# Kernel optimization log

Hardware: AMD Instinct MI355X
Metric: run time of the kernel (lower is better)

Reference implementation:

```python
import jax, jax.numpy as jnp
import numpy as np

E, R, K, D, B = 100000, 1000, 200, 256, 65536  # entities, relations, bundle heads, emb dim, batch


def setup_inputs() -> dict:
    key = jax.random.key(0)
    ks = jax.random.split(key, 12)
    ent_emb = jax.random.normal(ks[0], (E, D), dtype=jnp.float32)
    ent_emb = ent_emb / jnp.linalg.norm(ent_emb, axis=1, keepdims=True)  # xavier + L2 row-normalize
    heads = jax.random.normal(ks[1], (K, D), dtype=jnp.float32)
    heads = heads / jnp.linalg.norm(heads, axis=1, keepdims=True)  # normalize_vvrel_embeddings
    bases = jax.random.normal(ks[2], (R, 2, D), dtype=jnp.float32)
    bases = bases / jnp.linalg.norm(bases, axis=2, keepdims=True)  # normalize_all_rows
    rel2head = jax.random.randint(ks[3], (R,), 0, K)              # r_id2_vrr[rel][0] -> head idx
    rel2mult = jnp.where(jax.random.bernoulli(ks[4], 0.5, (R,)), 1.0, -1.0).astype(jnp.float32)  # r_id2_vrr[rel][1]
    return {
        'pos_h': jax.random.randint(ks[5], (B,), 0, E),
        'pos_t': jax.random.randint(ks[6], (B,), 0, E),
        'pos_r': jax.random.randint(ks[7], (B,), 0, R),
        'neg_h': jax.random.randint(ks[8], (B,), 0, E),
        'neg_t': jax.random.randint(ks[9], (B,), 0, E),
        'neg_r': jax.random.randint(ks[10], (B,), 0, R),
        'ent_emb': ent_emb, 'heads': heads, 'bases': bases,
        'rel2head': rel2head, 'rel2mult': rel2mult,
    }


def _transint_scores(pos_h, pos_t, pos_r, neg_h, neg_t, ent_emb, heads, bases, rel2head, rel2mult):
    # vvrel_embedding_func: head embedding scaled by +-1 multiplier
    r_e = heads[rel2head[pos_r]] * rel2mult[pos_r][:, None]           # [B, D]
    pos_sub = ent_emb[pos_h] + r_e - ent_emb[pos_t]                    # [B, D]
    neg_sub = ent_emb[neg_h] + r_e - ent_emb[neg_t]                    # [B, D] (note: uses pos_r_e, as in source)
    sub = jnp.concatenate([pos_sub, neg_sub], axis=0)                  # [2B, D]
    A = bases[jnp.concatenate([pos_r, pos_r], axis=0)]                 # [2B, 2, D] per-sample basis (comb_mats gather)
    # ATA and closed-form 2x2 inverse (module's `inverse`)
    ATA = jnp.einsum('bkd,bld->bkl', A, A)                             # [2B, 2, 2]
    a, b = ATA[:, 0, 0], ATA[:, 0, 1]
    c, d = ATA[:, 1, 0], ATA[:, 1, 1]
    det = a * d - b * c
    safe_det = jnp.where(det != 0, det, 1.0)
    inv_reg = jnp.stack([jnp.stack([d, -b], -1), jnp.stack([-c, a], -1)], -2) / safe_det[:, None, None]
    inv_fb = jnp.eye(2, dtype=ATA.dtype)[None] / a[:, None, None]      # fallback when det == 0
    ATA_inv = jnp.where((det != 0)[:, None, None], inv_reg, inv_fb)    # [2B, 2, 2]
    # P @ sub with P = I - A^T (A A^T)^{-1} A, applied without materializing P
    Asub = jnp.einsum('bkd,bd->bk', A, sub)                            # [2B, 2]
    proj = sub - jnp.einsum('bkd,bk->bd', A, jnp.einsum('bkl,bl->bk', ATA_inv, Asub))
    score = jnp.sum(proj ** 2, axis=1)                                 # L1_flag = False -> squared L2
    nb = pos_h.shape[0]
    return score[:nb], score[nb:]


def reference(pos_h, pos_t, pos_r, neg_h, neg_t, neg_r, ent_emb, heads, bases, rel2head, rel2mult):
    return _transint_scores(pos_h, pos_t, pos_r, neg_h, neg_t, ent_emb, heads, bases, rel2head, rel2mult)
```

## Files before the change

### kernel.cpp

```cpp
#include <hip/hip_runtime.h>

#define D 256
#define D4 (D/4)
#define RELQW 192

#define QSCALE (1.0f/254.0f)
#define QINV   254.0f
#define QS2    (QSCALE*QSCALE)

__device__ inline float dot4(const float4 u, const float4 v) {
    return u.x*v.x + u.y*v.y + u.z*v.z + u.w*v.w;
}

__device__ inline float wsum(float v) {
    #pragma unroll
    for (int off = 32; off > 0; off >>= 1)
        v += __shfl_xor(v, off, 64);
    return v;
}

__device__ inline void unpack_i8(unsigned w, int* f) {
    f[0] = (int)(w << 24) >> 24;
    f[1] = (int)(w << 16) >> 24;
    f[2] = (int)(w <<  8) >> 24;
    f[3] = (int)w         >> 24;
}

__device__ inline int q8(float v) {
    float q = rintf(v * QINV);
    q = fmaxf(-127.f, fminf(127.f, q));
    return (int)q;
}

__device__ inline unsigned pack4q(float a, float b, float c, float d) {
    return (unsigned)(q8(a) & 255)
         | ((unsigned)(q8(b) & 255) << 8)
         | ((unsigned)(q8(c) & 255) << 16)
         | ((unsigned)(q8(d) & 255) << 24);
}

__global__ __launch_bounds__(256) void transint_prep(
    const float*  __restrict__ ent,
    const float*  __restrict__ heads,
    const float*  __restrict__ bases,
    const int*    __restrict__ rel2head,
    const float*  __restrict__ rel2mult,
    unsigned*     __restrict__ ent_q,
    unsigned*     __restrict__ rel_q,
    float*        __restrict__ par_buf,
    int E, int R)
{
    const int wave = (blockIdx.x * blockDim.x + threadIdx.x) >> 6;
    const int lane = threadIdx.x & 63;

    if (wave < E) {
        float4 v = ((const float4*)ent)[(size_t)wave * D4 + lane];
        ent_q[(size_t)wave * 64 + lane] = pack4q(v.x, v.y, v.z, v.w);
        return;
    }
    const int r = wave - E;
    if (r >= R) return;

    const int hd = rel2head[r];
    const float mult = rel2mult[r];
    const float4* hrow = (const float4*)(heads + (size_t)hd * D);
    const float4* arow = (const float4*)(bases + (size_t)r * 2 * D);

    float4 a0 = arow[lane];
    float4 a1 = arow[D4 + lane];
    float4 re = hrow[lane];
    re.x *= mult; re.y *= mult; re.z *= mult; re.w *= mult;

    float aa = wsum(dot4(a0, a0));
    float ab = wsum(dot4(a0, a1));
    float dd = wsum(dot4(a1, a1));

    float det = aa * dd - ab * ab;
    float m00, m01, m11;
    if (det != 0.0f) {
        float inv = 1.0f / det;
        m00 = dd * inv; m01 = -ab * inv; m11 = aa * inv;
    } else {
        float inv = 1.0f / aa;
        m00 = inv; m01 = 0.0f; m11 = inv;
    }
    float t00 = aa * m00 + ab * m01;
    float t01 = aa * m01 + ab * m11;
    float t10 = ab * m00 + dd * m01;
    float t11 = ab * m01 + dd * m11;
    float q00 = 2.f * m00 - (m00 * t00 + m01 * t10);
    float q01 = 2.f * m01 - (m00 * t01 + m01 * t11);
    float q11 = 2.f * m11 - (m01 * t01 + m11 * t11);

    float c00 = sqrtf(aa);
    float ic00 = (c00 > 0.f) ? 1.f / c00 : 0.f;
    float4 u0;
    u0.x = a0.x * ic00; u0.y = a0.y * ic00; u0.z = a0.z * ic00; u0.w = a0.w * ic00;
    float c10 = ab * ic00;
    float4 v;
    v.x = a1.x - c10 * u0.x; v.y = a1.y - c10 * u0.y;
    v.z = a1.z - c10 * u0.z; v.w = a1.w - c10 * u0.w;
    float vv = wsum(dot4(v, v));
    float c11 = sqrtf(vv);
    float ic11 = (c11 > 0.f) ? 1.f / c11 : 0.f;
    float4 u1;
    u1.x = v.x * ic11; u1.y = v.y * ic11; u1.z = v.z * ic11; u1.w = v.w * ic11;

    float s00 = c00*c00*q00 + 2.f*c00*c10*q01 + c10*c10*q11;
    float s01 = c00*c11*q01 + c10*c11*q11;
    float s11 = c11*c11*q11;

    unsigned* base = rel_q + (size_t)r * RELQW;
    base[lane]       = pack4q(u0.x, u0.y, u0.z, u0.w);
    base[64 + lane]  = pack4q(u1.x, u1.y, u1.z, u1.w);
    base[128 + lane] = pack4q(re.x, re.y, re.z, re.w);

    if (lane == 0) {
        float* p = par_buf + (size_t)r * 4;
        p[0] = s00; p[1] = s01; p[2] = s11; p[3] = 0.f;
    }
}

__global__ __launch_bounds__(256) void transint_main(
    const int*      __restrict__ pos_h,
    const int*      __restrict__ pos_t,
    const int*      __restrict__ pos_r,
    const int*      __restrict__ neg_h,
    const int*      __restrict__ neg_t,
    const unsigned* __restrict__ ent_q,
    const unsigned* __restrict__ rel_q,
    const float*    __restrict__ par_buf,
    float*          __restrict__ out,
    int nB)
{
    const int wave = (blockIdx.x * blockDim.x + threadIdx.x) >> 6;
    const int lane = threadIdx.x & 63;
    const int g    = lane >> 4;
    const int gl   = lane & 15;
    const int base = wave * 8;
    int bs[2];
    bs[0] = base + g;
    bs[1] = base + 4 + g;
    if (bs[0] >= nB) return;
    const bool has1 = (bs[1] < nB);
    if (!has1) bs[1] = bs[0];

    const int4* eq = (const int4*)ent_q;
    const int4* rq = (const int4*)rel_q;

    int rr[2];
    const int4 *php[2], *ptp[2], *nhp[2], *ntp[2], *rbp[2];

    #pragma unroll
    for (int s = 0; s < 2; ++s) {
        const int b = bs[s];
        rr[s] = pos_r[b];
        php[s] = eq + (size_t)pos_h[b] * 16;
        ptp[s] = eq + (size_t)pos_t[b] * 16;
        nhp[s] = eq + (size_t)neg_h[b] * 16;
        ntp[s] = eq + (size_t)neg_t[b] * 16;
        rbp[s] = rq + (size_t)rr[s] * 48;
    }

    int pp0[2] = {0,0}, pp1[2] = {0,0};
    int pn0[2] = {0,0}, pn1[2] = {0,0};
    int ssp[2] = {0,0}, ssn[2] = {0,0};

    #pragma unroll
    for (int s = 0; s < 2; ++s) {
        int4 qh  = php[s][gl];
        int4 qt  = ptp[s][gl];
        int4 qx  = nhp[s][gl];
        int4 qy  = ntp[s][gl];
        int4 qu0 = rbp[s][gl];
        int4 qu1 = rbp[s][gl + 16];
        int4 qre = rbp[s][gl + 32];

        const unsigned* hw  = (const unsigned*)&qh;
        const unsigned* tw  = (const unsigned*)&qt;
        const unsigned* xw  = (const unsigned*)&qx;
        const unsigned* yw  = (const unsigned*)&qy;
        const unsigned* u0w = (const unsigned*)&qu0;
        const unsigned* u1w = (const unsigned*)&qu1;
        const unsigned* rw  = (const unsigned*)&qre;

        #pragma unroll
        for (int w = 0; w < 4; ++w) {
            int h4[4], t4[4], x4[4], y4[4], a4[4], b4[4], r4[4];
            unpack_i8(hw[w],  h4);
            unpack_i8(tw[w],  t4);
            unpack_i8(xw[w],  x4);
            unpack_i8(yw[w],  y4);
            unpack_i8(u0w[w], a4);
            unpack_i8(u1w[w], b4);
            unpack_i8(rw[w],  r4);
            #pragma unroll
            for (int j = 0; j < 4; ++j) {
                int ps = h4[j] - t4[j] + r4[j];
                int ns = x4[j] - y4[j] + r4[j];
                pp0[s] += a4[j] * ps;
                pp1[s] += b4[j] * ps;
                pn0[s] += a4[j] * ns;
                pn1[s] += b4[j] * ns;
                ssp[s] += ps * ps;
                ssn[s] += ns * ns;
            }
        }
    }

    #pragma unroll
    for (int off = 8; off > 0; off >>= 1) {
        #pragma unroll
        for (int s = 0; s < 2; ++s) {
            pp0[s] += __shfl_xor(pp0[s], off, 64);
            pp1[s] += __shfl_xor(pp1[s], off, 64);
            pn0[s] += __shfl_xor(pn0[s], off, 64);
            pn1[s] += __shfl_xor(pn1[s], off, 64);
            ssp[s] += __shfl_xor(ssp[s], off, 64);
            ssn[s] += __shfl_xor(ssn[s], off, 64);
        }
    }

    if (gl == 0) {
        #pragma unroll
        for (int s = 0; s < 2; ++s) {
            if (s == 1 && !has1) break;
            const float* par = par_buf + (size_t)rr[s] * 4;
            const float s00 = par[0], s01 = par[1], s11 = par[2];
            float P0 = (float)pp0[s] * QS2;
            float P1 = (float)pp1[s] * QS2;
            float N0 = (float)pn0[s] * QS2;
            float N1 = (float)pn1[s] * QS2;
            float SP = (float)ssp[s] * QS2;
            float SN = (float)ssn[s] * QS2;
            float sp = SP - (s00*P0*P0 + 2.f*s01*P0*P1 + s11*P1*P1);
            float sn = SN - (s00*N0*N0 + 2.f*s01*N0*N1 + s11*N1*N1);
            out[bs[s]]      = sp;
            out[nB + bs[s]] = sn;
        }
    }
}

extern "C" void kernel_launch(void* const* d_in, const int* in_sizes, int n_in,
                              void* d_out, int out_size, void* d_ws, size_t ws_size,
                              hipStream_t stream) {
    const int*   pos_h    = (const int*)  d_in[0];
    const int*   pos_t    = (const int*)  d_in[1];
    const int*   pos_r    = (const int*)  d_in[2];
    const int*   neg_h    = (const int*)  d_in[3];
    const int*   neg_t    = (const int*)  d_in[4];
    const float* ent_emb  = (const float*)d_in[6];
    const float* heads    = (const float*)d_in[7];
    const float* bases    = (const float*)d_in[8];
    const int*   rel2head = (const int*)  d_in[9];
    const float* rel2mult = (const float*)d_in[10];
    float* out = (float*)d_out;

    const int nB = in_sizes[0];
    const int R  = in_sizes[9];
    const int E  = in_sizes[6] / D;

    unsigned* ent_q   = (unsigned*)d_ws;
    unsigned* rel_q   = (unsigned*)((char*)d_ws + (size_t)E * 256);
    float*    par_buf = (float*)(rel_q + (size_t)R * RELQW);

    {
        int waves = E + R;
        dim3 grid((waves + 3) / 4);
        transint_prep<<<grid, dim3(256), 0, stream>>>(
            ent_emb, heads, bases, rel2head, rel2mult,
            ent_q, rel_q, par_buf, E, R);
    }
    {
        dim3 grid((nB + 31) / 32);
        transint_main<<<grid, dim3(256), 0, stream>>>(
            pos_h, pos_t, pos_r, neg_h, neg_t,
            ent_q, rel_q, par_buf, out, nB);
    }
}
```

Baseline: 187.6 us.

## Drop per-call int8 entity quantization and gather fp32 embeddings directly

The prep kernel no longer quantizes the whole 100k-row entity table to int8 on every call. It now only precomputes the orthonormal basis, relation vector and 2x2 correction terms per relation, stored in fp32. The main kernel gathers fp32 entity rows directly and accumulates in float, with one sample per 16-lane group. This removes a full read plus write pass over the entity table. In exchange, each gathered row is four times larger, so the random-gather traffic rises, and the kernel relies on the large last-level cache to hold the table.

```diff
diff --git a/kernel.cpp b/kernel.cpp
--- a/kernel.cpp
+++ b/kernel.cpp
@@ -2,11 +2,6 @@
 
 #define D 256
 #define D4 (D/4)
-#define RELQW 192
-
-#define QSCALE (1.0f/254.0f)
-#define QINV   254.0f
-#define QS2    (QSCALE*QSCALE)
 
 __device__ inline float dot4(const float4 u, const float4 v) {
     return u.x*v.x + u.y*v.y + u.z*v.z + u.w*v.w;
@@ -19,49 +14,20 @@
     return v;
 }
 
-__device__ inline void unpack_i8(unsigned w, int* f) {
-    f[0] = (int)(w << 24) >> 24;
-    f[1] = (int)(w << 16) >> 24;
-    f[2] = (int)(w <<  8) >> 24;
-    f[3] = (int)w         >> 24;
-}
-
-__device__ inline int q8(float v) {
-    float q = rintf(v * QINV);
-    q = fmaxf(-127.f, fminf(127.f, q));
-    return (int)q;
-}
-
-__device__ inline unsigned pack4q(float a, float b, float c, float d) {
-    return (unsigned)(q8(a) & 255)
-         | ((unsigned)(q8(b) & 255) << 8)
-         | ((unsigned)(q8(c) & 255) << 16)
-         | ((unsigned)(q8(d) & 255) << 24);
-}
-
-__global__ __launch_bounds__(256) void transint_prep(
-    const float*  __restrict__ ent,
-    const float*  __restrict__ heads,
-    const float*  __restrict__ bases,
-    const int*    __restrict__ rel2head,
-    const float*  __restrict__ rel2mult,
-    unsigned*     __restrict__ ent_q,
-    unsigned*     __restrict__ rel_q,
-    float*        __restrict__ par_buf,
-    int E, int R)
+__global__ __launch_bounds__(256) void transint_relprep(
+    const float* __restrict__ heads,
+    const float* __restrict__ bases,
+    const int*   __restrict__ rel2head,
+    const float* __restrict__ rel2mult,
+    float*       __restrict__ rel_f,
+    float*       __restrict__ par_buf,
+    int R)
 {
-    const int wave = (blockIdx.x * blockDim.x + threadIdx.x) >> 6;
+    const int r    = (blockIdx.x * blockDim.x + threadIdx.x) >> 6;
     const int lane = threadIdx.x & 63;
-
-    if (wave < E) {
-        float4 v = ((const float4*)ent)[(size_t)wave * D4 + lane];
-        ent_q[(size_t)wave * 64 + lane] = pack4q(v.x, v.y, v.z, v.w);
-        return;
-    }
-    const int r = wave - E;
     if (r >= R) return;
 
-    const int hd = rel2head[r];
+    const int   hd   = rel2head[r];
     const float mult = rel2mult[r];
     const float4* hrow = (const float4*)(heads + (size_t)hd * D);
     const float4* arow = (const float4*)(bases + (size_t)r * 2 * D);
@@ -92,7 +58,7 @@
     float q01 = 2.f * m01 - (m00 * t01 + m01 * t11);
     float q11 = 2.f * m11 - (m01 * t01 + m11 * t11);
 
-    float c00 = sqrtf(aa);
+    float c00  = sqrtf(aa);
     float ic00 = (c00 > 0.f) ? 1.f / c00 : 0.f;
     float4 u0;
     u0.x = a0.x * ic00; u0.y = a0.y * ic00; u0.z = a0.z * ic00; u0.w = a0.w * ic00;
@@ -100,8 +66,8 @@
     float4 v;
     v.x = a1.x - c10 * u0.x; v.y = a1.y - c10 * u0.y;
     v.z = a1.z - c10 * u0.z; v.w = a1.w - c10 * u0.w;
-    float vv = wsum(dot4(v, v));
-    float c11 = sqrtf(vv);
+    float vv   = wsum(dot4(v, v));
+    float c11  = sqrtf(vv);
     float ic11 = (c11 > 0.f) ? 1.f / c11 : 0.f;
     float4 u1;
     u1.x = v.x * ic11; u1.y = v.y * ic11; u1.z = v.z * ic11; u1.w = v.w * ic11;
@@ -110,10 +76,10 @@
     float s01 = c00*c11*q01 + c10*c11*q11;
     float s11 = c11*c11*q11;
 
-    unsigned* base = rel_q + (size_t)r * RELQW;
-    base[lane]       = pack4q(u0.x, u0.y, u0.z, u0.w);
-    base[64 + lane]  = pack4q(u1.x, u1.y, u1.z, u1.w);
-    base[128 + lane] = pack4q(re.x, re.y, re.z, re.w);
+    float4* rf = (float4*)(rel_f + (size_t)r * 3 * D);
+    rf[lane]          = u0;
+    rf[D4 + lane]     = u1;
+    rf[2 * D4 + lane] = re;
 
     if (lane == 0) {
         float* p = par_buf + (size_t)r * 4;
@@ -121,123 +87,78 @@
     }
 }
 
-__global__ __launch_bounds__(256) void transint_main(
-    const int*      __restrict__ pos_h,
-    const int*      __restrict__ pos_t,
-    const int*      __restrict__ pos_r,
-    const int*      __restrict__ neg_h,
-    const int*      __restrict__ neg_t,
-    const unsigned* __restrict__ ent_q,
-    const unsigned* __restrict__ rel_q,
-    const float*    __restrict__ par_buf,
-    float*          __restrict__ out,
+__global__ __launch_bounds__(256) void transint_main_f32(
+    const int*   __restrict__ pos_h,
+    const int*   __restrict__ pos_t,
+    const int*   __restrict__ pos_r,
+    const int*   __restrict__ neg_h,
+    const int*   __restrict__ neg_t,
+    const float* __restrict__ ent,
+    const float* __restrict__ rel_f,
+    const float* __restrict__ par_buf,
+    float*       __restrict__ out,
     int nB)
 {
     const int wave = (blockIdx.x * blockDim.x + threadIdx.x) >> 6;
     const int lane = threadIdx.x & 63;
     const int g    = lane >> 4;
     const int gl   = lane & 15;
-    const int base = wave * 8;
-    int bs[2];
-    bs[0] = base + g;
-    bs[1] = base + 4 + g;
-    if (bs[0] >= nB) return;
-    const bool has1 = (bs[1] < nB);
-    if (!has1) bs[1] = bs[0];
+    const int b    = wave * 4 + g;
+    if (b >= nB) return;
 
-    const int4* eq = (const int4*)ent_q;
-    const int4* rq = (const int4*)rel_q;
+    const int r = pos_r[b];
+    const float4* ph = (const float4*)ent + (size_t)pos_h[b] * D4;
+    const float4* pt = (const float4*)ent + (size_t)pos_t[b] * D4;
+    const float4* nh = (const float4*)ent + (size_t)neg_h[b] * D4;
+    const float4* nt = (const float4*)ent + (size_t)neg_t[b] * D4;
+    const float4* rb = (const float4*)rel_f + (size_t)r * (3 * D4);
 
-    int rr[2];
-    const int4 *php[2], *ptp[2], *nhp[2], *ntp[2], *rbp[2];
+    float4 H[4], T[4], X[4], Y[4], U0[4], U1[4], RE[4];
+    #pragma unroll
+    for (int c = 0; c < 4; ++c) {
+        const int fi = gl + 16 * c;
+        H[c]  = ph[fi];
+        T[c]  = pt[fi];
+        X[c]  = nh[fi];
+        Y[c]  = nt[fi];
+        U0[c] = rb[fi];
+        U1[c] = rb[D4 + fi];
+        RE[c] = rb[2 * D4 + fi];
+    }
+
+    float pp0 = 0.f, pp1 = 0.f, ssp = 0.f;
+    float pn0 = 0.f, pn1 = 0.f, ssn = 0.f;
 
     #pragma unroll
-    for (int s = 0; s < 2; ++s) {
-        const int b = bs[s];
-        rr[s] = pos_r[b];
-        php[s] = eq + (size_t)pos_h[b] * 16;
-        ptp[s] = eq + (size_t)pos_t[b] * 16;
-        nhp[s] = eq + (size_t)neg_h[b] * 16;
-        ntp[s] = eq + (size_t)neg_t[b] * 16;
-        rbp[s] = rq + (size_t)rr[s] * 48;
-    }
-
-    int pp0[2] = {0,0}, pp1[2] = {0,0};
-    int pn0[2] = {0,0}, pn1[2] = {0,0};
-    int ssp[2] = {0,0}, ssn[2] = {0,0};
-
-    #pragma unroll
-    for (int s = 0; s < 2; ++s) {
-        int4 qh  = php[s][gl];
-        int4 qt  = ptp[s][gl];
-        int4 qx  = nhp[s][gl];
-        int4 qy  = ntp[s][gl];
-        int4 qu0 = rbp[s][gl];
-        int4 qu1 = rbp[s][gl + 16];
-        int4 qre = rbp[s][gl + 32];
-
-        const unsigned* hw  = (const unsigned*)&qh;
-        const unsigned* tw  = (const unsigned*)&qt;
-        const unsigned* xw  = (const unsigned*)&qx;
-        const unsigned* yw  = (const unsigned*)&qy;
-        const unsigned* u0w = (const unsigned*)&qu0;
-        const unsigned* u1w = (const unsigned*)&qu1;
-        const unsigned* rw  = (const unsigned*)&qre;
-
-        #pragma unroll
-        for (int w = 0; w < 4; ++w) {
-            int h4[4], t4[4], x4[4], y4[4], a4[4], b4[4], r4[4];
-            unpack_i8(hw[w],  h4);
-            unpack_i8(tw[w],  t4);
-            unpack_i8(xw[w],  x4);
-            unpack_i8(yw[w],  y4);
-            unpack_i8(u0w[w], a4);
-            unpack_i8(u1w[w], b4);
-            unpack_i8(rw[w],  r4);
-            #pragma unroll
-            for (int j = 0; j < 4; ++j) {
-                int ps = h4[j] - t4[j] + r4[j];
-                int ns = x4[j] - y4[j] + r4[j];
-                pp0[s] += a4[j] * ps;
-                pp1[s] += b4[j] * ps;
-                pn0[s] += a4[j] * ns;
-                pn1[s] += b4[j] * ns;
-                ssp[s] += ps * ps;
-                ssn[s] += ns * ns;
-            }
-        }
+    for (int c = 0; c < 4; ++c) {
+        #define ACC(comp) {                                   \
+            float ps = H[c].comp - T[c].comp + RE[c].comp;    \
+            float ns = X[c].comp - Y[c].comp + RE[c].comp;    \
+            pp0 = fmaf(U0[c].comp, ps, pp0);                  \
+            pp1 = fmaf(U1[c].comp, ps, pp1);                  \
+            ssp = fmaf(ps, ps, ssp);                          \
+            pn0 = fmaf(U0[c].comp, ns, pn0);                  \
+            pn1 = fmaf(U1[c].comp, ns, pn1);                  \
+            ssn = fmaf(ns, ns, ssn); }
+        ACC(x) ACC(y) ACC(z) ACC(w)
+        #undef ACC
     }
 
     #pragma unroll
     for (int off = 8; off > 0; off >>= 1) {
-        #pragma unroll
-        for (int s = 0; s < 2; ++s) {
-            pp0[s] += __shfl_xor(pp0[s], off, 64);
-            pp1[s] += __shfl_xor(pp1[s], off, 64);
-            pn0[s] += __shfl_xor(pn0[s], off, 64);
-            pn1[s] += __shfl_xor(pn1[s], off, 64);
-            ssp[s] += __shfl_xor(ssp[s], off, 64);
-            ssn[s] += __shfl_xor(ssn[s], off, 64);
-        }
+        pp0 += __shfl_xor(pp0, off, 64);
+        pp1 += __shfl_xor(pp1, off, 64);
+        ssp += __shfl_xor(ssp, off, 64);
+        pn0 += __shfl_xor(pn0, off, 64);
+        pn1 += __shfl_xor(pn1, off, 64);
+        ssn += __shfl_xor(ssn, off, 64);
     }
 
     if (gl == 0) {
-        #pragma unroll
-        for (int s = 0; s < 2; ++s) {
-            if (s == 1 && !has1) break;
-            const float* par = par_buf + (size_t)rr[s] * 4;
-            const float s00 = par[0], s01 = par[1], s11 = par[2];
-            float P0 = (float)pp0[s] * QS2;
-            float P1 = (float)pp1[s] * QS2;
-            float N0 = (float)pn0[s] * QS2;
-            float N1 = (float)pn1[s] * QS2;
-            float SP = (float)ssp[s] * QS2;
-            float SN = (float)ssn[s] * QS2;
-            float sp = SP - (s00*P0*P0 + 2.f*s01*P0*P1 + s11*P1*P1);
-            float sn = SN - (s00*N0*N0 + 2.f*s01*N0*N1 + s11*N1*N1);
-            out[bs[s]]      = sp;
-            out[nB + bs[s]] = sn;
-        }
+        const float* par = par_buf + (size_t)r * 4;
+        const float s00 = par[0], s01 = par[1], s11 = par[2];
+        out[b]      = ssp - (s00*pp0*pp0 + 2.f*s01*pp0*pp1 + s11*pp1*pp1);
+        out[nB + b] = ssn - (s00*pn0*pn0 + 2.f*s01*pn0*pn1 + s11*pn1*pn1);
     }
 }
 
@@ -258,23 +179,19 @@
 
     const int nB = in_sizes[0];
     const int R  = in_sizes[9];
-    const int E  = in_sizes[6] / D;
 
-    unsigned* ent_q   = (unsigned*)d_ws;
-    unsigned* rel_q   = (unsigned*)((char*)d_ws + (size_t)E * 256);
-    float*    par_buf = (float*)(rel_q + (size_t)R * RELQW);
+    float* rel_f   = (float*)d_ws;
+    float* par_buf = rel_f + (size_t)R * 3 * D;
 
     {
-        int waves = E + R;
-        dim3 grid((waves + 3) / 4);
-        transint_prep<<<grid, dim3(256), 0, stream>>>(
-            ent_emb, heads, bases, rel2head, rel2mult,
-            ent_q, rel_q, par_buf, E, R);
+        dim3 grid((R + 3) / 4);
+        transint_relprep<<<grid, dim3(256), 0, stream>>>(
+            heads, bases, rel2head, rel2mult, rel_f, par_buf, R);
     }
     {
-        dim3 grid((nB + 31) / 32);
-        transint_main<<<grid, dim3(256), 0, stream>>>(
+        dim3 grid((nB + 15) / 16);
+        transint_main_f32<<<grid, dim3(256), 0, stream>>>(
             pos_h, pos_t, pos_r, neg_h, neg_t,
-            ent_q, rel_q, par_buf, out, nB);
+            ent_emb, rel_f, par_buf, out, nB);
     }
 }
```

New measurement: 197.0 us. 1.05x slower.

## Use packed int8 sdot4 dot products with precomputed relation cross terms

Applied to the files above, without the earlier changes.

Replaces the per-byte unpack and scalar multiply-accumulate in the main kernel with packed 4-way int8 dot products (sdot4). The squared norm and projections are expanded algebraically into pairwise dot products. The relation-only terms (u0·r, u1·r, r·r) are precomputed per relation in the prep kernel and stored in a widened parameter buffer. The intent is to cut ALU work in the main kernel. The cost is more sdot4 ops (18 per word instead of 6 sums) and a larger param row.

```diff
diff --git a/kernel.cpp b/kernel.cpp
--- a/kernel.cpp
+++ b/kernel.cpp
@@ -3,6 +3,7 @@
 #define D 256
 #define D4 (D/4)
 #define RELQW 192
+#define PARW 8
 
 #define QSCALE (1.0f/254.0f)
 #define QINV   254.0f
@@ -17,13 +18,6 @@
     for (int off = 32; off > 0; off >>= 1)
         v += __shfl_xor(v, off, 64);
     return v;
-}
-
-__device__ inline void unpack_i8(unsigned w, int* f) {
-    f[0] = (int)(w << 24) >> 24;
-    f[1] = (int)(w << 16) >> 24;
-    f[2] = (int)(w <<  8) >> 24;
-    f[3] = (int)w         >> 24;
 }
 
 __device__ inline int q8(float v) {
@@ -32,12 +26,33 @@
     return (int)q;
 }
 
+__device__ inline unsigned pack_i(const int* q) {
+    return (unsigned)(q[0] & 255)
+         | ((unsigned)(q[1] & 255) << 8)
+         | ((unsigned)(q[2] & 255) << 16)
+         | ((unsigned)(q[3] & 255) << 24);
+}
+
 __device__ inline unsigned pack4q(float a, float b, float c, float d) {
-    return (unsigned)(q8(a) & 255)
-         | ((unsigned)(q8(b) & 255) << 8)
-         | ((unsigned)(q8(c) & 255) << 16)
-         | ((unsigned)(q8(d) & 255) << 24);
-}
+    int q[4] = {q8(a), q8(b), q8(c), q8(d)};
+    return pack_i(q);
+}
+
+#if __has_builtin(__builtin_amdgcn_sdot4)
+__device__ inline int sdot4(int a, int b, int c) {
+    return __builtin_amdgcn_sdot4(a, b, c, false);
+}
+#else
+__device__ inline int sdot4(int a, int b, int c) {
+    #pragma unroll
+    for (int j = 0; j < 4; ++j) {
+        int av = (int)(((unsigned)a) << (24 - 8*j)) >> 24;
+        int bv = (int)(((unsigned)b) << (24 - 8*j)) >> 24;
+        c += av * bv;
+    }
+    return c;
+}
+#endif
 
 __global__ __launch_bounds__(256) void transint_prep(
     const float*  __restrict__ ent,
@@ -61,7 +76,7 @@
     const int r = wave - E;
     if (r >= R) return;
 
-    const int hd = rel2head[r];
+    const int   hd   = rel2head[r];
     const float mult = rel2mult[r];
     const float4* hrow = (const float4*)(heads + (size_t)hd * D);
     const float4* arow = (const float4*)(bases + (size_t)r * 2 * D);
@@ -92,7 +107,7 @@
     float q01 = 2.f * m01 - (m00 * t01 + m01 * t11);
     float q11 = 2.f * m11 - (m01 * t01 + m11 * t11);
 
-    float c00 = sqrtf(aa);
+    float c00  = sqrtf(aa);
     float ic00 = (c00 > 0.f) ? 1.f / c00 : 0.f;
     float4 u0;
     u0.x = a0.x * ic00; u0.y = a0.y * ic00; u0.z = a0.z * ic00; u0.w = a0.w * ic00;
@@ -100,8 +115,8 @@
     float4 v;
     v.x = a1.x - c10 * u0.x; v.y = a1.y - c10 * u0.y;
     v.z = a1.z - c10 * u0.z; v.w = a1.w - c10 * u0.w;
-    float vv = wsum(dot4(v, v));
-    float c11 = sqrtf(vv);
+    float vv   = wsum(dot4(v, v));
+    float c11  = sqrtf(vv);
     float ic11 = (c11 > 0.f) ? 1.f / c11 : 0.f;
     float4 u1;
     u1.x = v.x * ic11; u1.y = v.y * ic11; u1.z = v.z * ic11; u1.w = v.w * ic11;
@@ -110,14 +125,26 @@
     float s01 = c00*c11*q01 + c10*c11*q11;
     float s11 = c11*c11*q11;
 
-    unsigned* base = rel_q + (size_t)r * RELQW;
-    base[lane]       = pack4q(u0.x, u0.y, u0.z, u0.w);
-    base[64 + lane]  = pack4q(u1.x, u1.y, u1.z, u1.w);
-    base[128 + lane] = pack4q(re.x, re.y, re.z, re.w);
+    int qa[4] = {q8(u0.x), q8(u0.y), q8(u0.z), q8(u0.w)};
+    int qb[4] = {q8(u1.x), q8(u1.y), q8(u1.z), q8(u1.w)};
+    int qr[4] = {q8(re.x), q8(re.y), q8(re.z), q8(re.w)};
+
+    unsigned* basep = rel_q + (size_t)r * RELQW;
+    basep[lane]       = pack_i(qa);
+    basep[64 + lane]  = pack_i(qb);
+    basep[128 + lane] = pack_i(qr);
+
+    float du0re = wsum((float)(qa[0]*qr[0] + qa[1]*qr[1] + qa[2]*qr[2] + qa[3]*qr[3]));
+    float du1re = wsum((float)(qb[0]*qr[0] + qb[1]*qr[1] + qb[2]*qr[2] + qb[3]*qr[3]));
+    float drere = wsum((float)(qr[0]*qr[0] + qr[1]*qr[1] + qr[2]*qr[2] + qr[3]*qr[3]));
 
     if (lane == 0) {
-        float* p = par_buf + (size_t)r * 4;
-        p[0] = s00; p[1] = s01; p[2] = s11; p[3] = 0.f;
+        float* p = par_buf + (size_t)r * PARW;
+        p[0] = s00; p[1] = s01; p[2] = s11;
+        p[3] = du0re * QS2;
+        p[4] = du1re * QS2;
+        p[5] = drere * QS2;
+        p[6] = 0.f; p[7] = 0.f;
     }
 }
 
@@ -149,75 +176,70 @@
     const int4* rq = (const int4*)rel_q;
 
     int rr[2];
-    const int4 *php[2], *ptp[2], *nhp[2], *ntp[2], *rbp[2];
+    int4 qh[2], qt[2], qx[2], qy[2], qu0[2], qu1[2], qre[2];
 
     #pragma unroll
     for (int s = 0; s < 2; ++s) {
         const int b = bs[s];
         rr[s] = pos_r[b];
-        php[s] = eq + (size_t)pos_h[b] * 16;
-        ptp[s] = eq + (size_t)pos_t[b] * 16;
-        nhp[s] = eq + (size_t)neg_h[b] * 16;
-        ntp[s] = eq + (size_t)neg_t[b] * 16;
-        rbp[s] = rq + (size_t)rr[s] * 48;
-    }
-
-    int pp0[2] = {0,0}, pp1[2] = {0,0};
-    int pn0[2] = {0,0}, pn1[2] = {0,0};
-    int ssp[2] = {0,0}, ssn[2] = {0,0};
+        qh[s] = eq[(size_t)pos_h[b] * 16 + gl];
+        qt[s] = eq[(size_t)pos_t[b] * 16 + gl];
+        qx[s] = eq[(size_t)neg_h[b] * 16 + gl];
+        qy[s] = eq[(size_t)neg_t[b] * 16 + gl];
+        const int4* rb = rq + (size_t)rr[s] * 48;
+        qu0[s] = rb[gl];
+        qu1[s] = rb[gl + 16];
+        qre[s] = rb[gl + 32];
+    }
+
+    int p0[2], p1[2], sp[2], n0[2], n1[2], sn[2];
 
     #pragma unroll
     for (int s = 0; s < 2; ++s) {
-        int4 qh  = php[s][gl];
-        int4 qt  = ptp[s][gl];
-        int4 qx  = nhp[s][gl];
-        int4 qy  = ntp[s][gl];
-        int4 qu0 = rbp[s][gl];
-        int4 qu1 = rbp[s][gl + 16];
-        int4 qre = rbp[s][gl + 32];
-
-        const unsigned* hw  = (const unsigned*)&qh;
-        const unsigned* tw  = (const unsigned*)&qt;
-        const unsigned* xw  = (const unsigned*)&qx;
-        const unsigned* yw  = (const unsigned*)&qy;
-        const unsigned* u0w = (const unsigned*)&qu0;
-        const unsigned* u1w = (const unsigned*)&qu1;
-        const unsigned* rw  = (const unsigned*)&qre;
+        int u0h=0,u0t=0,u1h=0,u1t=0, hh=0,tt=0,ht=0, hre=0,tre=0;
+        int u0x=0,u0y=0,u1x=0,u1y=0, xx=0,yy=0,xy=0, xre=0,yre=0;
+
+        const int* hw  = (const int*)&qh[s];
+        const int* tw  = (const int*)&qt[s];
+        const int* xw  = (const int*)&qx[s];
+        const int* yw  = (const int*)&qy[s];
+        const int* aw  = (const int*)&qu0[s];
+        const int* bw  = (const int*)&qu1[s];
+        const int* rw  = (const int*)&qre[s];
 
         #pragma unroll
         for (int w = 0; w < 4; ++w) {
-            int h4[4], t4[4], x4[4], y4[4], a4[4], b4[4], r4[4];
-            unpack_i8(hw[w],  h4);
-            unpack_i8(tw[w],  t4);
-            unpack_i8(xw[w],  x4);
-            unpack_i8(yw[w],  y4);
-            unpack_i8(u0w[w], a4);
-            unpack_i8(u1w[w], b4);
-            unpack_i8(rw[w],  r4);
-            #pragma unroll
-            for (int j = 0; j < 4; ++j) {
-                int ps = h4[j] - t4[j] + r4[j];
-                int ns = x4[j] - y4[j] + r4[j];
-                pp0[s] += a4[j] * ps;
-                pp1[s] += b4[j] * ps;
-                pn0[s] += a4[j] * ns;
-                pn1[s] += b4[j] * ns;
-                ssp[s] += ps * ps;
-                ssn[s] += ns * ns;
-            }
+            const int h = hw[w], t = tw[w], x = xw[w], y = yw[w];
+            const int a = aw[w], b2 = bw[w], r2 = rw[w];
+            u0h = sdot4(a,  h, u0h);  u0t = sdot4(a,  t, u0t);
+            u1h = sdot4(b2, h, u1h);  u1t = sdot4(b2, t, u1t);
+            hh  = sdot4(h,  h, hh);   tt  = sdot4(t,  t, tt);
+            ht  = sdot4(h,  t, ht);
+            hre = sdot4(h, r2, hre);  tre = sdot4(t, r2, tre);
+            u0x = sdot4(a,  x, u0x);  u0y = sdot4(a,  y, u0y);
+            u1x = sdot4(b2, x, u1x);  u1y = sdot4(b2, y, u1y);
+            xx  = sdot4(x,  x, xx);   yy  = sdot4(y,  y, yy);
+            xy  = sdot4(x,  y, xy);
+            xre = sdot4(x, r2, xre);  yre = sdot4(y, r2, yre);
         }
+        p0[s] = u0h - u0t;
+        p1[s] = u1h - u1t;
+        sp[s] = hh + tt - 2*ht + 2*hre - 2*tre;
+        n0[s] = u0x - u0y;
+        n1[s] = u1x - u1y;
+        sn[s] = xx + yy - 2*xy + 2*xre - 2*yre;
     }
 
     #pragma unroll
     for (int off = 8; off > 0; off >>= 1) {
         #pragma unroll
         for (int s = 0; s < 2; ++s) {
-            pp0[s] += __shfl_xor(pp0[s], off, 64);
-            pp1[s] += __shfl_xor(pp1[s], off, 64);
-            pn0[s] += __shfl_xor(pn0[s], off, 64);
-            pn1[s] += __shfl_xor(pn1[s], off, 64);
-            ssp[s] += __shfl_xor(ssp[s], off, 64);
-            ssn[s] += __shfl_xor(ssn[s], off, 64);
+            p0[s] += __shfl_xor(p0[s], off, 64);
+            p1[s] += __shfl_xor(p1[s], off, 64);
+            sp[s] += __shfl_xor(sp[s], off, 64);
+            n0[s] += __shfl_xor(n0[s], off, 64);
+            n1[s] += __shfl_xor(n1[s], off, 64);
+            sn[s] += __shfl_xor(sn[s], off, 64);
         }
     }
 
@@ -225,18 +247,17 @@
         #pragma unroll
         for (int s = 0; s < 2; ++s) {
             if (s == 1 && !has1) break;
-            const float* par = par_buf + (size_t)rr[s] * 4;
+            const float* par = par_buf + (size_t)rr[s] * PARW;
             const float s00 = par[0], s01 = par[1], s11 = par[2];
-            float P0 = (float)pp0[s] * QS2;
-            float P1 = (float)pp1[s] * QS2;
-            float N0 = (float)pn0[s] * QS2;
-            float N1 = (float)pn1[s] * QS2;
-            float SP = (float)ssp[s] * QS2;
-            float SN = (float)ssn[s] * QS2;
-            float sp = SP - (s00*P0*P0 + 2.f*s01*P0*P1 + s11*P1*P1);
-            float sn = SN - (s00*N0*N0 + 2.f*s01*N0*N1 + s11*N1*N1);
-            out[bs[s]]      = sp;
-            out[nB + bs[s]] = sn;
+            const float u0re = par[3], u1re = par[4], rere = par[5];
+            float P0 = (float)p0[s] * QS2 + u0re;
+            float P1 = (float)p1[s] * QS2 + u1re;
+            float SP = (float)sp[s] * QS2 + rere;
+            float N0 = (float)n0[s] * QS2 + u0re;
+            float N1 = (float)n1[s] * QS2 + u1re;
+            float SN = (float)sn[s] * QS2 + rere;
+            out[bs[s]]      = SP - (s00*P0*P0 + 2.f*s01*P0*P1 + s11*P1*P1);
+            out[nB + bs[s]] = SN - (s00*N0*N0 + 2.f*s01*N0*N1 + s11*N1*N1);
         }
     }
 }
```

Result: no change. 186.5 us (median of 2 runs) (-0.6%).
